# Kernel optimization log

Hardware: AMD Instinct MI355X
Metric: run time of the kernel (lower is better)

Reference implementation:

```python
import jax, jax.numpy as jnp
import numpy as np

NUM_CODEBOOK = 2048
EMBED_DIM = 64
BETA = 0.25


def _l2norm(x, eps=1e-12):
    # F.normalize(x, dim=1): x / max(||x||, eps)
    n = jnp.sqrt(jnp.sum(x * x, axis=1, keepdims=True))
    return x / jnp.maximum(n, eps)


def setup_inputs() -> dict:
    key = jax.random.key(0)
    k1, k2 = jax.random.split(key)
    z = jax.random.normal(k1, (16, EMBED_DIM, 64, 64), dtype=jnp.float32)
    # xavier_normal_ init for (K, d) embedding weight
    std = float(np.sqrt(2.0 / (NUM_CODEBOOK + EMBED_DIM)))
    codebook = jax.random.normal(k2, (NUM_CODEBOOK, EMBED_DIM), dtype=jnp.float32) * std
    return {"z": z, "codebook": codebook}


def reference(z, codebook):
    b, d, h, w = z.shape
    z_bhwd = jnp.transpose(z, (0, 2, 3, 1))          # (b,h,w,d)
    z_flat = z_bhwd.reshape(-1, d)                   # (n,d)

    # normalize == 'l2'
    z_norm = _l2norm(z_flat)
    codebook_norm = _l2norm(codebook)                # (K,d)

    # squared euclidean distance: ||z||^2 + ||c||^2 - 2 z c^T  -> (n,K)
    distance = (jnp.sum(z_norm * z_norm, axis=1, keepdims=True)
                + jnp.sum(codebook_norm * codebook_norm, axis=1)
                - 2.0 * jnp.matmul(z_norm, codebook_norm.T))

    vq_indices = jnp.argmin(distance, axis=1)        # (n,)
    distance_prob = jax.nn.softmax(-distance, axis=1)

    z_q = codebook_norm[vq_indices]                  # (n,d) embedding gather

    codebook_loss = jnp.mean((z_q - jax.lax.stop_gradient(z_norm)) ** 2)
    commitment_loss = jnp.mean((z_norm - jax.lax.stop_gradient(z_q)) ** 2)
    loss = codebook_loss + BETA * commitment_loss

    # straight-through estimator
    z_q_st = z_norm + jax.lax.stop_gradient(z_q - z_norm)
    q = jnp.transpose(z_q_st.reshape(b, h, w, d), (0, 3, 1, 2))  # (b,d,h,w)
    return q, loss, codebook_loss, commitment_loss, distance_prob
```

## Files before the change

### kernel.cpp

```cpp
#include <hip/hip_runtime.h>

typedef _Float16 f16x8 __attribute__((ext_vector_type(8)));
typedef float f32x4 __attribute__((ext_vector_type(4)));

#define NN 65536
#define KK 2048
#define DD 64

__device__ __forceinline__ unsigned int fkey(float f) {
  unsigned int u = __float_as_uint(f);
  return (u & 0x80000000u) ? ~u : (u | 0x80000000u);
}

__global__ void k_norm_cb(const float* __restrict__ cb, float* __restrict__ cbT32,
                          float* __restrict__ cn2,
                          unsigned short* __restrict__ Bhi,
                          unsigned short* __restrict__ Blo) {
  int gid = blockIdx.x * blockDim.x + threadIdx.x;
  int c = gid >> 6;
  int k = gid & 63;
  float v = cb[c * DD + k];
  float ss = v * v;
  #pragma unroll
  for (int o = 32; o; o >>= 1) ss += __shfl_xor(ss, o);
  float inv = 1.0f / fmaxf(sqrtf(ss), 1e-12f);
  float cn = v * inv;
  cbT32[k * KK + c] = cn;
  float s2 = cn * cn;
  #pragma unroll
  for (int o = 32; o; o >>= 1) s2 += __shfl_xor(s2, o);
  if (k == 0) cn2[c] = s2;
  float sh = cn * 256.0f;
  _Float16 hh = (_Float16)sh;
  float resid = sh - (float)hh;
  _Float16 hl = (_Float16)(resid * 4096.0f);
  int s = k >> 5, g2 = (k >> 3) & 3, i = k & 7;
  int idx = s * 65536 + c * 32 + g2 * 8 + i;
  Bhi[idx] = *(unsigned short*)&hh;
  Blo[idx] = *(unsigned short*)&hl;
}

__global__ void k_norm_z(const float* __restrict__ z,
                         unsigned short* __restrict__ Ahi,
                         unsigned short* __restrict__ Alo) {
  __shared__ float np_[8][32];
  __shared__ float invS[32];
  int t = threadIdx.x;
  int r32 = t & 31, q = t >> 5;
  int n0 = blockIdx.x * 32;
  int w0 = n0 & 63, hh = (n0 >> 6) & 63, bb = n0 >> 12;
  const float* src = z + (size_t)bb * 262144 + (size_t)q * 8 * 4096 + hh * 64 + w0 + r32;
  float v[8];
  float ss = 0.f;
  #pragma unroll
  for (int i = 0; i < 8; ++i) {
    float x = src[(size_t)i * 4096];
    v[i] = x;
    ss = fmaf(x, x, ss);
  }
  np_[q][r32] = ss;
  __syncthreads();
  if (t < 32) {
    float s = 0.f;
    #pragma unroll
    for (int qq = 0; qq < 8; ++qq) s += np_[qq][t];
    invS[t] = 1.0f / fmaxf(sqrtf(s), 1e-12f);
  }
  __syncthreads();
  float inv = invS[r32] * 256.0f;
  union { _Float16 h[8]; uint4 u; } hi, lo;
  #pragma unroll
  for (int i = 0; i < 8; ++i) {
    float sh = v[i] * inv;
    _Float16 a = (_Float16)sh;
    hi.h[i] = a;
    lo.h[i] = (_Float16)((sh - (float)a) * 4096.0f);
  }
  int rt = (n0 + r32) >> 4;
  int r = r32 & 15;
  int s = q >> 2, g2 = q & 3;
  size_t idx = (size_t)(rt * 2 + s) * 64 + g2 * 16 + r;
  ((uint4*)Ahi)[idx] = hi.u;
  ((uint4*)Alo)[idx] = lo.u;
}

__global__ __launch_bounds__(1024) void k_main(
    const f16x8* __restrict__ Ahi, const f16x8* __restrict__ Alo,
    const f16x8* __restrict__ Bhi, const f16x8* __restrict__ Blo,
    const float* __restrict__ cn2g, const float* __restrict__ cbT32,
    float* __restrict__ qout, float* __restrict__ prob,
    float* __restrict__ partials) {
  __shared__ unsigned long long keyS[16];
  __shared__ float rowpart[16][16];
  __shared__ float rowInv[16];
  __shared__ float wsum[16];

  int t = threadIdx.x;
  int lane = t & 63, wv = t >> 6;
  int l15 = lane & 15, g = lane >> 4;
  int rt = blockIdx.x;
  int n0 = rt * 16;
  int wc0 = wv * 128;

  if (t < 16) keyS[t] = ~0ull;

  f16x8 z_hi[2], z_lo[2];
  {
    size_t base = (size_t)rt * 128 + (size_t)g * 16 + l15;
    z_hi[0] = Ahi[base];      z_hi[1] = Ahi[base + 64];
    z_lo[0] = Alo[base];      z_lo[1] = Alo[base + 64];
  }

  f32x4 acc1[8], acc2[8];
  #pragma unroll
  for (int i = 0; i < 8; ++i) {
    acc1[i] = (f32x4){0.f, 0.f, 0.f, 0.f};
    acc2[i] = (f32x4){0.f, 0.f, 0.f, 0.f};
  }

  int b0 = (wc0 + l15) * 4 + g;
  f16x8 bhA = Bhi[b0], blA = Blo[b0];
  f16x8 bhB, blB;
  #pragma unroll
  for (int p = 0; p < 16; ++p) {
    int t8 = p >> 1, s = p & 1;
    if (p < 15) {
      int pn = p + 1;
      int idxn = (pn & 1) * 8192 + (pn >> 1) * 64 + b0;
      if (p & 1) { bhA = Bhi[idxn]; blA = Blo[idxn]; }
      else       { bhB = Bhi[idxn]; blB = Blo[idxn]; }
    }
    f16x8 bh = (p & 1) ? bhB : bhA;
    f16x8 bl = (p & 1) ? blB : blA;
    acc2[t8] = __builtin_amdgcn_mfma_f32_16x16x32_f16(bh, z_lo[s], acc2[t8], 0, 0, 0);
    acc1[t8] = __builtin_amdgcn_mfma_f32_16x16x32_f16(bh, z_hi[s], acc1[t8], 0, 0, 0);
    acc2[t8] = __builtin_amdgcn_mfma_f32_16x16x32_f16(bl, z_hi[s], acc2[t8], 0, 0, 0);
  }

  unsigned long long kmin = ~0ull;
  float esum = 0.f;
  int cb0 = wc0 + g * 4;
  #pragma unroll
  for (int t8 = 0; t8 < 8; ++t8) {
    int c0 = cb0 + t8 * 16;
    float4 c4 = *(const float4*)(cn2g + c0);
    float cn[4] = {c4.x, c4.y, c4.z, c4.w};
    #pragma unroll
    for (int r = 0; r < 4; ++r) {
      float dot = fmaf(acc2[t8][r], 3.7252903e-09f, acc1[t8][r] * 1.52587890625e-05f);
      float d = fmaf(-2.0f, dot, cn[r]);
      unsigned long long kk = ((unsigned long long)fkey(d) << 32) | (unsigned)(c0 + r);
      if (kk < kmin) kmin = kk;
      float e = __expf(-d);
      acc1[t8][r] = e;
      esum += e;
    }
  }
  #pragma unroll
  for (int o = 16; o <= 32; o <<= 1) {
    esum += __shfl_xor(esum, o);
    unsigned long long ok = __shfl_xor(kmin, o);
    if (ok < kmin) kmin = ok;
  }
  __syncthreads();
  if (lane < 16) {
    rowpart[l15][wv] = esum;
    atomicMin(&keyS[l15], kmin);
  }
  __syncthreads();
  if (t < 16) {
    float s = 0.f;
    #pragma unroll
    for (int w = 0; w < 16; ++w) s += rowpart[t][w];
    rowInv[t] = 1.0f / s;
  }
  __syncthreads();

  {
    float inv = rowInv[l15];
    float* pp = prob + (size_t)(n0 + l15) * KK + cb0;
    #pragma unroll
    for (int t8 = 0; t8 < 8; ++t8) {
      f32x4 o4 = acc1[t8] * inv;
      *(f32x4*)(pp + t8 * 16) = o4;
    }
  }

  {
    int r = t & 15, k = t >> 4;
    int cw = (int)(keyS[r] & 0xffffffffull);
    float qv = cbT32[k * KK + cw];
    int w0 = n0 & 63, hh2 = (n0 >> 6) & 63, bb = n0 >> 12;
    qout[((size_t)((bb << 6) | k) * 64 + hh2) * 64 + w0 + r] = qv;
    size_t aidx = ((size_t)(rt * 2 + (k >> 5)) * 64 + ((k >> 3) & 3) * 16 + r) * 8 + (k & 7);
    float ah = (float)((const _Float16*)Ahi)[aidx];
    float al = (float)((const _Float16*)Alo)[aidx];
    float zn = fmaf(al, 2.44140625e-04f, ah) * 3.90625e-03f;
    float df = qv - zn;
    float ssd = df * df;
    #pragma unroll
    for (int o = 32; o; o >>= 1) ssd += __shfl_xor(ssd, o);
    if (lane == 0) wsum[wv] = ssd;
  }
  __syncthreads();
  if (t == 0) {
    float s = 0.f;
    #pragma unroll
    for (int w = 0; w < 16; ++w) s += wsum[w];
    partials[rt] = s;
  }
}

__global__ void k_final(const float* __restrict__ partials, float* __restrict__ out) {
  __shared__ float wsh[4];
  int t = threadIdx.x;
  float s = 0.f;
  for (int i = 0; i < 16; ++i) s += partials[t * 16 + i];
  #pragma unroll
  for (int o = 32; o; o >>= 1) s += __shfl_xor(s, o);
  if ((t & 63) == 0) wsh[t >> 6] = s;
  __syncthreads();
  if (t == 0) {
    float tot = (wsh[0] + wsh[1]) + (wsh[2] + wsh[3]);
    float cbl = tot * (1.0f / 4194304.0f);
    out[4194304] = 1.25f * cbl;
    out[4194305] = cbl;
    out[4194306] = cbl;
  }
}

extern "C" void kernel_launch(void* const* d_in, const int* in_sizes, int n_in,
                              void* d_out, int out_size, void* d_ws, size_t ws_size,
                              hipStream_t stream) {
  const float* z = (const float*)d_in[0];
  const float* cb = (const float*)d_in[1];
  float* out = (float*)d_out;
  char* ws = (char*)d_ws;

  float* cbT32 = (float*)(ws);
  float* cn2 = (float*)(ws + 524288);
  unsigned short* Bhi = (unsigned short*)(ws + 532480);
  unsigned short* Blo = (unsigned short*)(ws + 794624);
  float* partials = (float*)(ws + 1056768);
  unsigned short* Ahi = (unsigned short*)(ws + 1073152);
  unsigned short* Alo = (unsigned short*)(ws + 9461760);

  k_norm_cb<<<512, 256, 0, stream>>>(cb, cbT32, cn2, Bhi, Blo);
  k_norm_z<<<2048, 256, 0, stream>>>(z, Ahi, Alo);
  k_main<<<4096, 1024, 0, stream>>>((const f16x8*)Ahi, (const f16x8*)Alo,
                                    (const f16x8*)Bhi, (const f16x8*)Blo,
                                    cn2, cbT32, out, out + 4194307, partials);
  k_final<<<1, 256, 0, stream>>>(partials, out);
}
```

Baseline: 317.4 us.

## Halve k_main block size, two codebook passes with fp16 LDS staging of exps

k_main now runs 512 threads per block, so each wave covers two 1024-codeword halves in sequence. The first half's exponentials are kept in shared memory as fp16 until the row sum is known. The lo-correction accumulator is folded into the main accumulator after every k-step, which removes the second 8-entry accumulator array and cuts register pressure. Together with launch_bounds(512,4) this aims at higher occupancy, with more serial work per wave and some LDS traffic as the cost. Storing the first-half probabilities through fp16 lowers their precision.

```diff
diff --git a/kernel.cpp b/kernel.cpp
--- a/kernel.cpp
+++ b/kernel.cpp
@@ -1,4 +1,5 @@
 #include <hip/hip_runtime.h>
+#include <hip/hip_fp16.h>
 
 typedef _Float16 f16x8 __attribute__((ext_vector_type(8)));
 typedef float f32x4 __attribute__((ext_vector_type(4)));
@@ -84,23 +85,23 @@
   ((uint4*)Alo)[idx] = lo.u;
 }
 
-__global__ __launch_bounds__(1024) void k_main(
+__global__ __launch_bounds__(512, 4) void k_main(
     const f16x8* __restrict__ Ahi, const f16x8* __restrict__ Alo,
     const f16x8* __restrict__ Bhi, const f16x8* __restrict__ Blo,
     const float* __restrict__ cn2g, const float* __restrict__ cbT32,
     float* __restrict__ qout, float* __restrict__ prob,
     float* __restrict__ partials) {
+  __shared__ __half ehS[16][1032];
   __shared__ unsigned long long keyS[16];
-  __shared__ float rowpart[16][16];
+  __shared__ float rowpart[16][8];
   __shared__ float rowInv[16];
-  __shared__ float wsum[16];
+  __shared__ float wsum[8];
 
   int t = threadIdx.x;
   int lane = t & 63, wv = t >> 6;
   int l15 = lane & 15, g = lane >> 4;
   int rt = blockIdx.x;
   int n0 = rt * 16;
-  int wc0 = wv * 128;
 
   if (t < 16) keyS[t] = ~0ull;
 
@@ -111,93 +112,123 @@
     z_lo[0] = Alo[base];      z_lo[1] = Alo[base + 64];
   }
 
-  f32x4 acc1[8], acc2[8];
-  #pragma unroll
-  for (int i = 0; i < 8; ++i) {
-    acc1[i] = (f32x4){0.f, 0.f, 0.f, 0.f};
-    acc2[i] = (f32x4){0.f, 0.f, 0.f, 0.f};
-  }
-
-  int b0 = (wc0 + l15) * 4 + g;
-  f16x8 bhA = Bhi[b0], blA = Blo[b0];
-  f16x8 bhB, blB;
-  #pragma unroll
-  for (int p = 0; p < 16; ++p) {
-    int t8 = p >> 1, s = p & 1;
-    if (p < 15) {
-      int pn = p + 1;
-      int idxn = (pn & 1) * 8192 + (pn >> 1) * 64 + b0;
-      if (p & 1) { bhA = Bhi[idxn]; blA = Blo[idxn]; }
-      else       { bhB = Bhi[idxn]; blB = Blo[idxn]; }
-    }
-    f16x8 bh = (p & 1) ? bhB : bhA;
-    f16x8 bl = (p & 1) ? blB : blA;
-    acc2[t8] = __builtin_amdgcn_mfma_f32_16x16x32_f16(bh, z_lo[s], acc2[t8], 0, 0, 0);
-    acc1[t8] = __builtin_amdgcn_mfma_f32_16x16x32_f16(bh, z_hi[s], acc1[t8], 0, 0, 0);
-    acc2[t8] = __builtin_amdgcn_mfma_f32_16x16x32_f16(bl, z_hi[s], acc2[t8], 0, 0, 0);
-  }
-
+  f32x4 acc1[8];
   unsigned long long kmin = ~0ull;
-  float esum = 0.f;
-  int cb0 = wc0 + g * 4;
-  #pragma unroll
-  for (int t8 = 0; t8 < 8; ++t8) {
-    int c0 = cb0 + t8 * 16;
-    float4 c4 = *(const float4*)(cn2g + c0);
-    float cn[4] = {c4.x, c4.y, c4.z, c4.w};
-    #pragma unroll
-    for (int r = 0; r < 4; ++r) {
-      float dot = fmaf(acc2[t8][r], 3.7252903e-09f, acc1[t8][r] * 1.52587890625e-05f);
-      float d = fmaf(-2.0f, dot, cn[r]);
-      unsigned long long kk = ((unsigned long long)fkey(d) << 32) | (unsigned)(c0 + r);
-      if (kk < kmin) kmin = kk;
-      float e = __expf(-d);
-      acc1[t8][r] = e;
-      esum += e;
-    }
-  }
+  float esumT = 0.f;
+
+  #pragma unroll
+  for (int pass = 0; pass < 2; ++pass) {
+    int wc0 = pass * 1024 + wv * 128;
+    #pragma unroll
+    for (int i = 0; i < 8; ++i) acc1[i] = (f32x4){0.f, 0.f, 0.f, 0.f};
+    f32x4 acc2t = (f32x4){0.f, 0.f, 0.f, 0.f};
+
+    int b0 = (wc0 + l15) * 4 + g;
+    f16x8 bhA = Bhi[b0], blA = Blo[b0];
+    f16x8 bhB, blB;
+    #pragma unroll
+    for (int p = 0; p < 16; ++p) {
+      int t8 = p >> 1, s = p & 1;
+      if (p < 15) {
+        int pn = p + 1;
+        int idxn = (pn & 1) * 8192 + (pn >> 1) * 64 + b0;
+        if (p & 1) { bhA = Bhi[idxn]; blA = Blo[idxn]; }
+        else       { bhB = Bhi[idxn]; blB = Blo[idxn]; }
+      }
+      f16x8 bh = (p & 1) ? bhB : bhA;
+      f16x8 bl = (p & 1) ? blB : blA;
+      acc2t    = __builtin_amdgcn_mfma_f32_16x16x32_f16(bh, z_lo[s], acc2t, 0, 0, 0);
+      acc1[t8] = __builtin_amdgcn_mfma_f32_16x16x32_f16(bh, z_hi[s], acc1[t8], 0, 0, 0);
+      acc2t    = __builtin_amdgcn_mfma_f32_16x16x32_f16(bl, z_hi[s], acc2t, 0, 0, 0);
+      if (s == 1) {
+        acc1[t8] += acc2t * 2.44140625e-04f;
+        acc2t = (f32x4){0.f, 0.f, 0.f, 0.f};
+      }
+    }
+
+    int cb0 = wc0 + g * 4;
+    #pragma unroll
+    for (int t8 = 0; t8 < 8; ++t8) {
+      int c0 = cb0 + t8 * 16;
+      float4 c4 = *(const float4*)(cn2g + c0);
+      float cn[4] = {c4.x, c4.y, c4.z, c4.w};
+      #pragma unroll
+      for (int r = 0; r < 4; ++r) {
+        float d = fmaf(acc1[t8][r], -3.0517578125e-05f, cn[r]);
+        unsigned long long kk = ((unsigned long long)fkey(d) << 32) | (unsigned)(c0 + r);
+        if (kk < kmin) kmin = kk;
+        float e = __expf(-d);
+        acc1[t8][r] = e;
+        esumT += e;
+      }
+    }
+    if (pass == 0) {
+      #pragma unroll
+      for (int t8 = 0; t8 < 8; ++t8) {
+        int off = wv * 128 + t8 * 16 + g * 4;
+        *(__half2*)&ehS[l15][off]     = __floats2half2_rn(acc1[t8][0], acc1[t8][1]);
+        *(__half2*)&ehS[l15][off + 2] = __floats2half2_rn(acc1[t8][2], acc1[t8][3]);
+      }
+    }
+  }
+
   #pragma unroll
   for (int o = 16; o <= 32; o <<= 1) {
-    esum += __shfl_xor(esum, o);
+    esumT += __shfl_xor(esumT, o);
     unsigned long long ok = __shfl_xor(kmin, o);
     if (ok < kmin) kmin = ok;
   }
   __syncthreads();
   if (lane < 16) {
-    rowpart[l15][wv] = esum;
+    rowpart[l15][wv] = esumT;
     atomicMin(&keyS[l15], kmin);
   }
   __syncthreads();
   if (t < 16) {
     float s = 0.f;
     #pragma unroll
-    for (int w = 0; w < 16; ++w) s += rowpart[t][w];
+    for (int w = 0; w < 8; ++w) s += rowpart[t][w];
     rowInv[t] = 1.0f / s;
   }
   __syncthreads();
 
   {
     float inv = rowInv[l15];
-    float* pp = prob + (size_t)(n0 + l15) * KK + cb0;
+    float* pr = prob + (size_t)(n0 + l15) * KK + wv * 128 + g * 4;
+    #pragma unroll
+    for (int t8 = 0; t8 < 8; ++t8)
+      *(f32x4*)(pr + 1024 + t8 * 16) = acc1[t8] * inv;
     #pragma unroll
     for (int t8 = 0; t8 < 8; ++t8) {
-      f32x4 o4 = acc1[t8] * inv;
-      *(f32x4*)(pp + t8 * 16) = o4;
+      int off = wv * 128 + t8 * 16 + g * 4;
+      __half2 a = *(__half2*)&ehS[l15][off];
+      __half2 b = *(__half2*)&ehS[l15][off + 2];
+      f32x4 o4;
+      o4[0] = __low2float(a) * inv;
+      o4[1] = __high2float(a) * inv;
+      o4[2] = __low2float(b) * inv;
+      o4[3] = __high2float(b) * inv;
+      *(f32x4*)(pr + t8 * 16) = o4;
     }
   }
 
   {
-    int r = t & 15, k = t >> 4;
-    int cw = (int)(keyS[r] & 0xffffffffull);
-    float qv = cbT32[k * KK + cw];
-    int w0 = n0 & 63, hh2 = (n0 >> 6) & 63, bb = n0 >> 12;
-    qout[((size_t)((bb << 6) | k) * 64 + hh2) * 64 + w0 + r] = qv;
-    size_t aidx = ((size_t)(rt * 2 + (k >> 5)) * 64 + ((k >> 3) & 3) * 16 + r) * 8 + (k & 7);
-    float ah = (float)((const _Float16*)Ahi)[aidx];
-    float al = (float)((const _Float16*)Alo)[aidx];
-    float zn = fmaf(al, 2.44140625e-04f, ah) * 3.90625e-03f;
-    float df = qv - zn;
-    float ssd = df * df;
+    float ssd = 0.f;
+    #pragma unroll
+    for (int i = 0; i < 2; ++i) {
+      int e = i * 512 + t;
+      int d = e >> 4, wi = e & 15;
+      int cw = (int)(keyS[wi] & 0xffffffffull);
+      float qv = cbT32[d * KK + cw];
+      int w0 = n0 & 63, hh2 = (n0 >> 6) & 63, bb = n0 >> 12;
+      qout[((size_t)((bb << 6) | d) * 64 + hh2) * 64 + w0 + wi] = qv;
+      size_t aidx = ((size_t)(rt * 2 + (d >> 5)) * 64 + ((d >> 3) & 3) * 16 + wi) * 8 + (d & 7);
+      float ah = (float)((const _Float16*)Ahi)[aidx];
+      float al = (float)((const _Float16*)Alo)[aidx];
+      float zn = fmaf(al, 2.44140625e-04f, ah) * 3.90625e-03f;
+      float df = qv - zn;
+      ssd = fmaf(df, df, ssd);
+    }
     #pragma unroll
     for (int o = 32; o; o >>= 1) ssd += __shfl_xor(ssd, o);
     if (lane == 0) wsum[wv] = ssd;
@@ -206,7 +237,7 @@
   if (t == 0) {
     float s = 0.f;
     #pragma unroll
-    for (int w = 0; w < 16; ++w) s += wsum[w];
+    for (int w = 0; w < 8; ++w) s += wsum[w];
     partials[rt] = s;
   }
 }
@@ -247,8 +278,8 @@
 
   k_norm_cb<<<512, 256, 0, stream>>>(cb, cbT32, cn2, Bhi, Blo);
   k_norm_z<<<2048, 256, 0, stream>>>(z, Ahi, Alo);
-  k_main<<<4096, 1024, 0, stream>>>((const f16x8*)Ahi, (const f16x8*)Alo,
-                                    (const f16x8*)Bhi, (const f16x8*)Blo,
-                                    cn2, cbT32, out, out + 4194307, partials);
+  k_main<<<4096, 512, 0, stream>>>((const f16x8*)Ahi, (const f16x8*)Alo,
+                                   (const f16x8*)Bhi, (const f16x8*)Blo,
+                                   cn2, cbT32, out, out + 4194307, partials);
   k_final<<<1, 256, 0, stream>>>(partials, out);
 }
```

After: 289.9 us. -8.7%, faster.
